# Kernel optimization log

Measured on AMD Instinct MI355X. Metric: run time of the kernel, lower is better.

## Reference

```python
import jax, jax.numpy as jnp
import numpy as np

B, S, D, H = 2, 2048, 2048, 16
DK = D // H  # 128


def _rope(x, cos, sin):
    # x: [B,S,H,DK]; pairs (x0,x1),(x2,x3),... rotated as complex numbers
    xr = x[..., 0::2]  # [B,S,H,DK/2]
    xi = x[..., 1::2]
    yr = xr * cos - xi * sin
    yi = xr * sin + xi * cos
    y = jnp.stack([yr, yi], axis=-1)  # [B,S,H,DK/2,2]
    return y.reshape(x.shape)


def setup_inputs() -> dict:
    key = jax.random.key(0)
    ks = jax.random.split(key, 12)
    sc = 1.0 / np.sqrt(D)
    q = jax.random.normal(ks[0], (B, S, D), jnp.float32)
    k = jax.random.normal(ks[1], (B, S, D), jnp.float32)
    v = jax.random.normal(ks[2], (B, S, D), jnp.float32)
    mask = jnp.tril(jnp.ones((S, S), jnp.int32))[None, None]  # causal [1,1,S,S]
    # standard RoPE angles: pos * theta^(-2i/dk)
    theta = 10000.0 ** (-jnp.arange(0, DK, 2, dtype=jnp.float32) / DK)  # [DK/2]
    freqs_angles = jnp.arange(S, dtype=jnp.float32)[:, None] * theta[None, :]  # [S,DK/2]
    wq = jax.random.normal(ks[3], (D, D), jnp.float32) * sc
    bq = jax.random.normal(ks[4], (D,), jnp.float32) * 0.01
    wk = jax.random.normal(ks[5], (D, D), jnp.float32) * sc
    bk = jax.random.normal(ks[6], (D,), jnp.float32) * 0.01
    wv = jax.random.normal(ks[7], (D, D), jnp.float32) * sc
    bv = jax.random.normal(ks[8], (D,), jnp.float32) * 0.01
    wo = jax.random.normal(ks[9], (D, D), jnp.float32) * sc
    bo = jax.random.normal(ks[10], (D,), jnp.float32) * 0.01
    return dict(q=q, k=k, v=v, mask=mask, freqs_angles=freqs_angles,
                wq=wq, bq=bq, wk=wk, bk=bk, wv=wv, bv=bv, wo=wo, bo=bo)


def reference(q, k, v, mask, freqs_angles, wq, bq, wk, bk, wv, bv, wo, bo):
    query = q @ wq.T + bq
    key_ = k @ wk.T + bk
    value = v @ wv.T + bv
    query = query.reshape(B, S, H, DK)
    key_ = key_.reshape(B, S, H, DK)
    value = value.reshape(B, S, H, DK).transpose(0, 2, 1, 3)  # [B,H,S,DK]
    cos = jnp.cos(freqs_angles)[None, :, None, :]  # [1,S,1,DK/2]
    sin = jnp.sin(freqs_angles)[None, :, None, :]
    query = _rope(query, cos, sin).transpose(0, 2, 1, 3)  # [B,H,S,DK]
    key_ = _rope(key_, cos, sin).transpose(0, 2, 1, 3)
    scores = jnp.einsum('bhqd,bhkd->bhqk', query, key_) / jnp.sqrt(jnp.float32(DK))
    scores = jnp.where(mask == 0, jnp.float32(-1e9), scores)
    attn = jax.nn.softmax(scores, axis=-1)  # dropout p=0.0 -> identity
    x = jnp.einsum('bhqk,bhkd->bhqd', attn, value)
    x = x.transpose(0, 2, 1, 3).reshape(B, S, D)
    return x @ wo.T + bo
```

## Files before the change

### kernel.cpp

```cpp
#include <hip/hip_runtime.h>
#include <hip/hip_bf16.h>

#define BB 2
#define SS 2048
#define DD 2048
#define HH 16
#define DKK 128
#define MM (BB*SS)

typedef unsigned short u16;
typedef short bf16x8 __attribute__((ext_vector_type(8)));
typedef unsigned short u16x8 __attribute__((ext_vector_type(8)));
typedef float f32x4 __attribute__((ext_vector_type(4)));

static __device__ __forceinline__ f32x4 mfma_bf16(bf16x8 a, bf16x8 b, f32x4 c) {
  return __builtin_amdgcn_mfma_f32_16x16x32_bf16(a, b, c, 0, 0, 0);
}

static __device__ __forceinline__ u16 f2b(float f) {
  unsigned int u = __float_as_uint(f);
  u = (u + 0x7FFFu + ((u >> 16) & 1u)) >> 16;
  return (u16)u;
}

static __device__ __forceinline__ u16 f2bq(float f) {
  unsigned int r;
  asm("v_cvt_pk_bf16_f32 %0, %1, %2" : "=v"(r) : "v"(f), "v"(f));
  return (u16)r;
}

static __device__ __forceinline__ void gl16(const u16* g, u16* l) {
  __builtin_amdgcn_global_load_lds(
      (const __attribute__((address_space(1))) unsigned int*)(const void*)g,
      (__attribute__((address_space(3))) unsigned int*)(void*)l, 16, 0, 0);
}

struct F2BArgs { const float* src[7]; u16* dst[7]; const float* fa; float* cs; };
__global__ __launch_bounds__(256) void k_f2bf_all(F2BArgs a) {
  int bid = blockIdx.x;
  if (bid >= 20480) {
    const int t0 = ((bid - 20480) * 256 + threadIdx.x) * 8;
    float4 a0 = *reinterpret_cast<const float4*>(a.fa + t0);
    float4 a1 = *reinterpret_cast<const float4*>(a.fa + t0 + 4);
    float4 o0, o1, o2, o3;
    o0.x = cosf(a0.x); o0.y = sinf(a0.x); o0.z = cosf(a0.y); o0.w = sinf(a0.y);
    o1.x = cosf(a0.z); o1.y = sinf(a0.z); o1.z = cosf(a0.w); o1.w = sinf(a0.w);
    o2.x = cosf(a1.x); o2.y = sinf(a1.x); o2.z = cosf(a1.y); o2.w = sinf(a1.y);
    o3.x = cosf(a1.z); o3.y = sinf(a1.z); o3.z = cosf(a1.w); o3.w = sinf(a1.w);
    float* out = a.cs + 2 * t0;
    *reinterpret_cast<float4*>(out)      = o0;
    *reinterpret_cast<float4*>(out + 4)  = o1;
    *reinterpret_cast<float4*>(out + 8)  = o2;
    *reinterpret_cast<float4*>(out + 12) = o3;
    return;
  }
  int buf, local;
  if (bid < 12288) { buf = bid >> 12; local = bid & 4095; }
  else { int t = bid - 12288; buf = 3 + (t >> 11); local = t & 2047; }
  const int i = (local * 256 + threadIdx.x) * 8;
  const float* in = a.src[buf];
  float4 v0 = *reinterpret_cast<const float4*>(in + i);
  float4 v1 = *reinterpret_cast<const float4*>(in + i + 4);
  u16x8 o;
  o[0]=f2b(v0.x); o[1]=f2b(v0.y); o[2]=f2b(v0.z); o[3]=f2b(v0.w);
  o[4]=f2b(v1.x); o[5]=f2b(v1.y); o[6]=f2b(v1.z); o[7]=f2b(v1.w);
  *reinterpret_cast<u16x8*>(a.dst[buf] + i) = o;
}

struct GemmJob { const u16* A; const u16* W; const float* bias; void* out; int mode; };
struct GemmArgs { GemmJob job[3]; };
__global__ __launch_bounds__(256, 2) void k_gemm(GemmArgs ga, const float* __restrict__ cs) {
  const GemmJob J = ga.job[blockIdx.z];
  const u16* __restrict__ A = J.A;
  const u16* __restrict__ W = J.W;
  const int mode = J.mode;
  const int K = DD, N = DD;

  __shared__ __align__(16) u16 sA[128 * 64];
  __shared__ __align__(16) u16 sB[256 * 64];
  const int tid = threadIdx.x;
  const int l  = tid & 63;
  const int w  = tid >> 6;
  const int wr = w >> 1;
  const int wc = w & 1;
  const int bm = blockIdx.x * 128, bn = blockIdx.y * 256;
  const int lr = l & 15;
  const int lg = l >> 4;

  f32x4 acc[4][8];
#pragma unroll
  for (int mi = 0; mi < 4; mi++)
#pragma unroll
    for (int ni = 0; ni < 8; ni++)
#pragma unroll
      for (int j = 0; j < 4; j++) acc[mi][ni][j] = 0.0f;

  const int srcx = ((l & 7) * 8) ^ ((l >> 3) * 8);
  const u16* gAl = A + (size_t)(bm + w*32 + (l >> 3)) * K + srcx;
  const u16* gBl = W + (size_t)(bn + w*64 + (l >> 3)) * K + srcx;

  const int rx = (lr & 7) * 8;

  for (int k0 = 0; k0 < K; k0 += 64) {
    __syncthreads();
#pragma unroll
    for (int i = 0; i < 4; i++) gl16(gAl + (size_t)i*8*K + k0, sA + (w*32 + i*8) * 64);
#pragma unroll
    for (int i = 0; i < 8; i++) gl16(gBl + (size_t)i*8*K + k0, sB + (w*64 + i*8) * 64);
    __syncthreads();

#pragma unroll
    for (int kk = 0; kk < 2; kk++) {
      bf16x8 af[4], bfv[8];
#pragma unroll
      for (int i = 0; i < 4; i++)
        af[i]  = *reinterpret_cast<const bf16x8*>(
            sA + (wr*64 + i*16 + lr) * 64 + ((kk*32 + lg*8) ^ rx));
#pragma unroll
      for (int i = 0; i < 8; i++)
        bfv[i] = *reinterpret_cast<const bf16x8*>(
            sB + (wc*128 + i*16 + lr) * 64 + ((kk*32 + lg*8) ^ rx));
#pragma unroll
      for (int mi = 0; mi < 4; mi++)
#pragma unroll
        for (int ni = 0; ni < 8; ni++)
          acc[mi][ni] = mfma_bf16(af[mi], bfv[ni], acc[mi][ni]);
    }
  }

#pragma unroll
  for (int mi = 0; mi < 4; mi++) {
#pragma unroll
    for (int ni = 0; ni < 8; ni++) {
      const int col = bn + wc*128 + ni*16 + lr;
      const float bv = J.bias[col];
#pragma unroll
      for (int r = 0; r < 4; r++) {
        const int row = bm + wr*64 + mi*16 + lg*4 + r;
        float v = acc[mi][ni][r] + bv;
        if (mode & 1) {
          const int s  = row & (SS - 1);
          const int dk = col & (DKK - 1);
          const int p  = dk >> 1;
          const float2 csv = *reinterpret_cast<const float2*>(cs + (size_t)(s*64 + p)*2);
          const float other = __shfl_xor(v, 1);
          const float sgn = (dk & 1) ? csv.y : -csv.y;
          v = v * csv.x + other * sgn;
          if (mode == 3) v *= 0.12751744f;
        }
        if (mode == 2) {
          reinterpret_cast<float*>(J.out)[(size_t)row * N + col] = v;
        } else {
          reinterpret_cast<u16*>(J.out)[(size_t)row * N + col] = f2b(v);
        }
      }
    }
  }
}

__global__ __launch_bounds__(256, 1) void k_attn(const u16* __restrict__ Qp,
                                                 const u16* __restrict__ Kp,
                                                 const u16* __restrict__ Vp,
                                                 u16* __restrict__ Op) {
  const int bid = blockIdx.x;
  const int qt = 15 - (bid >> 5);
  const int bh = bid & 31;
  const int h  = bh & 15;
  const int b  = bh >> 4;
  const int tid = threadIdx.x;
  const int l  = tid & 63, w = tid >> 6;
  const int lr = l & 15, lg = l >> 4;

  __shared__ __align__(16) u16 Klds[2 * 128 * 128];
  __shared__ __align__(16) u16 VT[128 * 128];
  __shared__ __align__(16) u16 PL[4][32][136];

  int koff[8];
#pragma unroll
  for (int i = 0; i < 8; i++) {
    const int row = w*32 + i*4 + (l >> 4);
    koff[i] = row * DD + (((l & 15) * 8) ^ ((row & 7) * 8));
  }
  const u16* kbase = Kp + (size_t)b * SS * DD + h * DKK;

  const int k0v = (tid >> 4) * 8;
  const int d0  = (tid & 15) * 8;
  const u16* vbase = Vp + (size_t)b * SS * DD + h * DKK + (size_t)k0v * DD + d0;

  uint4 vr[8];

  auto stageK = [&](int nk, int bufq) {
    const u16* kb = kbase + (size_t)nk * (128 * DD);
    u16* dst = Klds + bufq * 16384 + (w * 32) * 128;
#pragma unroll
    for (int i = 0; i < 8; i++) gl16(kb + koff[i], dst + i * 512);
  };
  auto prefV = [&](int nk) {
    const u16* vb = vbase + (size_t)nk * (128 * DD);
#pragma unroll
    for (int c = 0; c < 8; c++) vr[c] = *reinterpret_cast<const uint4*>(vb + c * DD);
  };

  int cur = 0;
  stageK(0, 0);
  prefV(0);

  bf16x8 qf[2][4];
#pragma unroll
  for (int mt = 0; mt < 2; mt++) {
    const size_t qrow = (size_t)(b*SS + qt*128 + w*32 + mt*16 + lr) * DD + h*DKK;
#pragma unroll
    for (int kk = 0; kk < 4; kk++)
      qf[mt][kk] = *reinterpret_cast<const bf16x8*>(Qp + qrow + kk*32 + lg*8);
  }

  float m[2][4], lsum[2][4];
  f32x4 oacc[2][8];
#pragma unroll
  for (int mt = 0; mt < 2; mt++)
#pragma unroll
    for (int r = 0; r < 4; r++) { m[mt][r] = -INFINITY; lsum[mt][r] = 0.0f; }
#pragma unroll
  for (int mt = 0; mt < 2; mt++)
#pragma unroll
    for (int dt = 0; dt < 8; dt++)
#pragma unroll
      for (int jj = 0; jj < 4; jj++) oacc[mt][dt][jj] = 0.0f;

#pragma unroll 1
  for (int kv = 0; kv <= qt; kv++) {
    __syncthreads();
#pragma unroll
    for (int dj = 0; dj < 8; dj++) {
      const int row = d0 + dj;
      const int col = k0v ^ (((row ^ (row >> 3)) & 15) * 8);
      u16x8 pk;
#pragma unroll
      for (int j = 0; j < 8; j++) pk[j] = reinterpret_cast<const u16*>(&vr[j])[dj];
      *reinterpret_cast<u16x8*>(VT + row * 128 + col) = pk;
    }
    __syncthreads();

    const bool hasnext = (kv < qt);
    if (hasnext) {
      prefV(kv + 1);
      stageK(kv + 1, cur ^ 1);
    }

    f32x4 sa[2][8];
#pragma unroll
    for (int mt = 0; mt < 2; mt++)
#pragma unroll
      for (int kt = 0; kt < 8; kt++)
#pragma unroll
        for (int jj = 0; jj < 4; jj++) sa[mt][kt][jj] = 0.0f;
    const u16* kl = Klds + cur * 16384;
    __builtin_amdgcn_s_setprio(1);
#pragma unroll
    for (int kk = 0; kk < 4; kk++) {
#pragma unroll
      for (int kt = 0; kt < 8; kt++) {
        const int row = kt*16 + lr;
        const bf16x8 kf = *reinterpret_cast<const bf16x8*>(
            kl + row * 128 + ((kk*32 + lg*8) ^ ((row & 7) * 8)));
#pragma unroll
        for (int mt = 0; mt < 2; mt++)
          sa[mt][kt] = mfma_bf16(qf[mt][kk], kf, sa[mt][kt]);
      }
    }
    __builtin_amdgcn_s_setprio(0);

    if (kv == qt) {
#pragma unroll
      for (int kt = 0; kt < 8; kt++) {
        const int key = kv*128 + kt*16 + lr;
#pragma unroll
        for (int mt = 0; mt < 2; mt++)
#pragma unroll
          for (int r = 0; r < 4; r++) {
            const int qv = qt*128 + w*32 + mt*16 + lg*4 + r;
            if (key > qv) sa[mt][kt][r] = -1e9f;
          }
      }
    }

    float pm[2][4];
#pragma unroll
    for (int mt = 0; mt < 2; mt++)
#pragma unroll
      for (int r = 0; r < 4; r++) {
        float t0 = fmaxf(fmaxf(sa[mt][0][r], sa[mt][1][r]), fmaxf(sa[mt][2][r], sa[mt][3][r]));
        float t1 = fmaxf(fmaxf(sa[mt][4][r], sa[mt][5][r]), fmaxf(sa[mt][6][r], sa[mt][7][r]));
        pm[mt][r] = fmaxf(t0, t1);
      }
    bool ok = true;
#pragma unroll
    for (int mt = 0; mt < 2; mt++)
#pragma unroll
      for (int r = 0; r < 4; r++) ok = ok && (pm[mt][r] <= m[mt][r] + 8.0f);
    if (!__all(ok)) {
#pragma unroll
      for (int mt = 0; mt < 2; mt++)
#pragma unroll
        for (int r = 0; r < 4; r++) {
          float t = pm[mt][r];
#pragma unroll
          for (int d = 1; d < 16; d <<= 1) t = fmaxf(t, __shfl_xor(t, d));
          const float mnew = fmaxf(m[mt][r], t);
          const float corr = exp2f(m[mt][r] - mnew);
          lsum[mt][r] *= corr;
#pragma unroll
          for (int dt = 0; dt < 8; dt++) oacc[mt][dt][r] *= corr;
          m[mt][r] = mnew;
        }
    }

#pragma unroll
    for (int mt = 0; mt < 2; mt++)
#pragma unroll
      for (int r = 0; r < 4; r++) {
        float rs = 0.0f;
#pragma unroll
        for (int kt = 0; kt < 8; kt++) {
          const float e = exp2f(sa[mt][kt][r] - m[mt][r]);
          rs += e;
          PL[w][mt*16 + lg*4 + r][kt*16 + lr] = f2bq(e);
        }
        lsum[mt][r] += rs;
      }

    __builtin_amdgcn_s_setprio(1);
#pragma unroll
    for (int kk2 = 0; kk2 < 4; kk2++) {
      bf16x8 pa[2];
#pragma unroll
      for (int mt = 0; mt < 2; mt++)
        pa[mt] = *reinterpret_cast<const bf16x8*>(&PL[w][mt*16 + lr][kk2*32 + lg*8]);
#pragma unroll
      for (int dt = 0; dt < 8; dt++) {
        const int row = dt*16 + lr;
        const bf16x8 vb = *reinterpret_cast<const bf16x8*>(
            VT + row * 128 + ((kk2*32 + lg*8) ^ (((row ^ (row >> 3)) & 15) * 8)));
#pragma unroll
        for (int mt = 0; mt < 2; mt++)
          oacc[mt][dt] = mfma_bf16(pa[mt], vb, oacc[mt][dt]);
      }
    }
    __builtin_amdgcn_s_setprio(0);

    if (hasnext) cur ^= 1;
  }

  float inv[2][4];
#pragma unroll
  for (int mt = 0; mt < 2; mt++)
#pragma unroll
    for (int r = 0; r < 4; r++) {
      float t = lsum[mt][r];
#pragma unroll
      for (int d = 1; d < 16; d <<= 1) t += __shfl_xor(t, d);
      inv[mt][r] = 1.0f / t;
    }
#pragma unroll
  for (int mt = 0; mt < 2; mt++)
#pragma unroll
    for (int dt = 0; dt < 8; dt++)
#pragma unroll
      for (int r = 0; r < 4; r++) {
        const size_t row = (size_t)(b*SS + qt*128 + w*32 + mt*16 + lg*4 + r);
        Op[row * DD + h*DKK + dt*16 + lr] = f2bq(oacc[mt][dt][r] * inv[mt][r]);
      }
}

extern "C" void kernel_launch(void* const* d_in, const int* in_sizes, int n_in,
                              void* d_out, int out_size, void* d_ws, size_t ws_size,
                              hipStream_t stream) {
  const float* q  = (const float*)d_in[0];
  const float* k  = (const float*)d_in[1];
  const float* v  = (const float*)d_in[2];
  const float* fa = (const float*)d_in[4];
  const float* wq = (const float*)d_in[5];
  const float* bq = (const float*)d_in[6];
  const float* wk = (const float*)d_in[7];
  const float* bk = (const float*)d_in[8];
  const float* wv = (const float*)d_in[9];
  const float* bv = (const float*)d_in[10];
  const float* wo = (const float*)d_in[11];
  const float* bo = (const float*)d_in[12];

  float* cs = (float*)d_ws;
  u16* bf = (u16*)((char*)d_ws + (size_t)262144 * sizeof(float));
  const size_t NX = (size_t)MM * DD;
  const size_t NW = (size_t)DD * DD;
  u16* q_bf  = bf;
  u16* k_bf  = q_bf + NX;
  u16* v_bf  = k_bf + NX;
  u16* wq_bf = v_bf + NX;
  u16* wk_bf = wq_bf + NW;
  u16* wv_bf = wk_bf + NW;
  u16* wo_bf = wv_bf + NW;
  u16* Qp    = wo_bf + NW;
  u16* Kp    = Qp + NX;
  u16* Vp    = Kp + NX;
  u16* Ao    = Vp + NX;

  F2BArgs fa7;
  fa7.src[0] = q;  fa7.dst[0] = q_bf;
  fa7.src[1] = k;  fa7.dst[1] = k_bf;
  fa7.src[2] = v;  fa7.dst[2] = v_bf;
  fa7.src[3] = wq; fa7.dst[3] = wq_bf;
  fa7.src[4] = wk; fa7.dst[4] = wk_bf;
  fa7.src[5] = wv; fa7.dst[5] = wv_bf;
  fa7.src[6] = wo; fa7.dst[6] = wo_bf;
  fa7.fa = fa;     fa7.cs = cs;
  k_f2bf_all<<<dim3(20544), 256, 0, stream>>>(fa7);

  GemmArgs gq;
  gq.job[0] = GemmJob{ q_bf, wq_bf, bq, (void*)Qp, 3 };
  gq.job[1] = GemmJob{ k_bf, wk_bf, bk, (void*)Kp, 1 };
  gq.job[2] = GemmJob{ v_bf, wv_bf, bv, (void*)Vp, 0 };
  k_gemm<<<dim3(MM/128, DD/256, 3), 256, 0, stream>>>(gq, cs);

  k_attn<<<dim3(512), 256, 0, stream>>>(Qp, Kp, Vp, Ao);

  GemmArgs go;
  go.job[0] = GemmJob{ Ao, wo_bf, bo, d_out, 2 };
  go.job[1] = go.job[0];
  go.job[2] = go.job[0];
  k_gemm<<<dim3(MM/128, DD/256, 1), 256, 0, stream>>>(go, cs);
}
```

Measured before the change: 344.8 us.

## Halve attention KV tile, raise occupancy, reorder blocks, add 128x128 output GEMM

The attention kernel now processes 64-key tiles instead of 128, cutting LDS and register use so two blocks can share a CU (launch bounds 2). Blocks are split into heavy-first and light-first halves to balance the causal workload. The output projection switches to a new 128x128-tile GEMM, which launches twice as many blocks for better CU fill. The trade-off is more loop iterations and barriers per attention block, and less data reuse per tile in the output GEMM.

```diff
diff --git a/kernel.cpp b/kernel.cpp
--- a/kernel.cpp
+++ b/kernel.cpp
@@ -69,6 +69,7 @@
 
 struct GemmJob { const u16* A; const u16* W; const float* bias; void* out; int mode; };
 struct GemmArgs { GemmJob job[3]; };
+
 __global__ __launch_bounds__(256, 2) void k_gemm(GemmArgs ga, const float* __restrict__ cs) {
   const GemmJob J = ga.job[blockIdx.z];
   const u16* __restrict__ A = J.A;
@@ -158,47 +159,136 @@
   }
 }
 
-__global__ __launch_bounds__(256, 1) void k_attn(const u16* __restrict__ Qp,
+__global__ __launch_bounds__(256) void k_gemm3(GemmArgs ga, const float* __restrict__ cs) {
+  const GemmJob J = ga.job[blockIdx.z];
+  const u16* __restrict__ A = J.A;
+  const u16* __restrict__ W = J.W;
+  const int mode = J.mode;
+  const int K = DD, N = DD;
+
+  __shared__ __align__(16) u16 sA[128 * 64];
+  __shared__ __align__(16) u16 sB[128 * 64];
+  const int tid = threadIdx.x;
+  const int l  = tid & 63;
+  const int w  = tid >> 6;
+  const int wr = w >> 1, wc = w & 1;
+  const int bm = blockIdx.x * 128, bn = blockIdx.y * 128;
+  const int lr = l & 15;
+  const int lg = l >> 4;
+
+  f32x4 acc[4][4];
+#pragma unroll
+  for (int mi = 0; mi < 4; mi++)
+#pragma unroll
+    for (int ni = 0; ni < 4; ni++)
+#pragma unroll
+      for (int j = 0; j < 4; j++) acc[mi][ni][j] = 0.0f;
+
+  const int srcx = ((l & 7) * 8) ^ ((l >> 3) * 8);
+  const u16* gAl = A + (size_t)(bm + w*32 + (l >> 3)) * K + srcx;
+  const u16* gBl = W + (size_t)(bn + w*32 + (l >> 3)) * K + srcx;
+
+  const int rx = (lr & 7) * 8;
+
+  for (int k0 = 0; k0 < K; k0 += 64) {
+    __syncthreads();
+#pragma unroll
+    for (int i = 0; i < 4; i++) gl16(gAl + (size_t)i*8*K + k0, sA + (w*32 + i*8) * 64);
+#pragma unroll
+    for (int i = 0; i < 4; i++) gl16(gBl + (size_t)i*8*K + k0, sB + (w*32 + i*8) * 64);
+    __syncthreads();
+
+#pragma unroll
+    for (int kk = 0; kk < 2; kk++) {
+      bf16x8 af[4], bfv[4];
+#pragma unroll
+      for (int i = 0; i < 4; i++)
+        af[i]  = *reinterpret_cast<const bf16x8*>(
+            sA + (wr*64 + i*16 + lr) * 64 + ((kk*32 + lg*8) ^ rx));
+#pragma unroll
+      for (int i = 0; i < 4; i++)
+        bfv[i] = *reinterpret_cast<const bf16x8*>(
+            sB + (wc*64 + i*16 + lr) * 64 + ((kk*32 + lg*8) ^ rx));
+#pragma unroll
+      for (int mi = 0; mi < 4; mi++)
+#pragma unroll
+        for (int ni = 0; ni < 4; ni++)
+          acc[mi][ni] = mfma_bf16(af[mi], bfv[ni], acc[mi][ni]);
+    }
+  }
+
+#pragma unroll
+  for (int mi = 0; mi < 4; mi++) {
+#pragma unroll
+    for (int ni = 0; ni < 4; ni++) {
+      const int col = bn + wc*64 + ni*16 + lr;
+      const float bv = J.bias[col];
+#pragma unroll
+      for (int r = 0; r < 4; r++) {
+        const int row = bm + wr*64 + mi*16 + lg*4 + r;
+        float v = acc[mi][ni][r] + bv;
+        if (mode & 1) {
+          const int s  = row & (SS - 1);
+          const int dk = col & (DKK - 1);
+          const int p  = dk >> 1;
+          const float2 csv = *reinterpret_cast<const float2*>(cs + (size_t)(s*64 + p)*2);
+          const float other = __shfl_xor(v, 1);
+          const float sgn = (dk & 1) ? csv.y : -csv.y;
+          v = v * csv.x + other * sgn;
+          if (mode == 3) v *= 0.12751744f;
+        }
+        if (mode == 2) {
+          reinterpret_cast<float*>(J.out)[(size_t)row * N + col] = v;
+        } else {
+          reinterpret_cast<u16*>(J.out)[(size_t)row * N + col] = f2b(v);
+        }
+      }
+    }
+  }
+}
+
+__global__ __launch_bounds__(256, 2) void k_attn(const u16* __restrict__ Qp,
                                                  const u16* __restrict__ Kp,
                                                  const u16* __restrict__ Vp,
                                                  u16* __restrict__ Op) {
   const int bid = blockIdx.x;
-  const int qt = 15 - (bid >> 5);
-  const int bh = bid & 31;
+  int bh, qt;
+  if (bid < 256) { bh = bid & 31; qt = 15 - (bid >> 5); }
+  else { int b2 = bid - 256; bh = b2 & 31; qt = b2 >> 5; }
   const int h  = bh & 15;
   const int b  = bh >> 4;
   const int tid = threadIdx.x;
   const int l  = tid & 63, w = tid >> 6;
   const int lr = l & 15, lg = l >> 4;
 
-  __shared__ __align__(16) u16 Klds[2 * 128 * 128];
-  __shared__ __align__(16) u16 VT[128 * 128];
-  __shared__ __align__(16) u16 PL[4][32][136];
-
-  int koff[8];
-#pragma unroll
-  for (int i = 0; i < 8; i++) {
-    const int row = w*32 + i*4 + (l >> 4);
+  __shared__ __align__(16) u16 Klds[2 * 64 * 128];
+  __shared__ __align__(16) u16 VT[128 * 64];
+  __shared__ __align__(16) u16 PL[4][32][72];
+
+  int koff[4];
+#pragma unroll
+  for (int i = 0; i < 4; i++) {
+    const int row = w*16 + i*4 + (l >> 4);
     koff[i] = row * DD + (((l & 15) * 8) ^ ((row & 7) * 8));
   }
   const u16* kbase = Kp + (size_t)b * SS * DD + h * DKK;
 
-  const int k0v = (tid >> 4) * 8;
-  const int d0  = (tid & 15) * 8;
+  const int k0v = (tid >> 5) * 8;
+  const int d0  = (tid & 31) * 4;
   const u16* vbase = Vp + (size_t)b * SS * DD + h * DKK + (size_t)k0v * DD + d0;
 
-  uint4 vr[8];
+  uint2 vr[8];
 
   auto stageK = [&](int nk, int bufq) {
-    const u16* kb = kbase + (size_t)nk * (128 * DD);
-    u16* dst = Klds + bufq * 16384 + (w * 32) * 128;
-#pragma unroll
-    for (int i = 0; i < 8; i++) gl16(kb + koff[i], dst + i * 512);
+    const u16* kb = kbase + (size_t)nk * (64 * DD);
+    u16* dst = Klds + bufq * 8192 + (w * 16) * 128;
+#pragma unroll
+    for (int i = 0; i < 4; i++) gl16(kb + koff[i], dst + i * 512);
   };
   auto prefV = [&](int nk) {
-    const u16* vb = vbase + (size_t)nk * (128 * DD);
-#pragma unroll
-    for (int c = 0; c < 8; c++) vr[c] = *reinterpret_cast<const uint4*>(vb + c * DD);
+    const u16* vb = vbase + (size_t)nk * (64 * DD);
+#pragma unroll
+    for (int c = 0; c < 8; c++) vr[c] = *reinterpret_cast<const uint2*>(vb + c * DD);
   };
 
   int cur = 0;
@@ -227,39 +317,40 @@
 #pragma unroll
       for (int jj = 0; jj < 4; jj++) oacc[mt][dt][jj] = 0.0f;
 
+  const int kvmax = 2 * qt + 1;
 #pragma unroll 1
-  for (int kv = 0; kv <= qt; kv++) {
+  for (int kv = 0; kv <= kvmax; kv++) {
     __syncthreads();
 #pragma unroll
-    for (int dj = 0; dj < 8; dj++) {
+    for (int dj = 0; dj < 4; dj++) {
       const int row = d0 + dj;
-      const int col = k0v ^ (((row ^ (row >> 3)) & 15) * 8);
+      const int col = k0v ^ (((row ^ (row >> 3)) & 7) * 8);
       u16x8 pk;
 #pragma unroll
       for (int j = 0; j < 8; j++) pk[j] = reinterpret_cast<const u16*>(&vr[j])[dj];
-      *reinterpret_cast<u16x8*>(VT + row * 128 + col) = pk;
+      *reinterpret_cast<u16x8*>(VT + row * 64 + col) = pk;
     }
     __syncthreads();
 
-    const bool hasnext = (kv < qt);
+    const bool hasnext = (kv < kvmax);
     if (hasnext) {
       prefV(kv + 1);
       stageK(kv + 1, cur ^ 1);
     }
 
-    f32x4 sa[2][8];
+    f32x4 sa[2][4];
 #pragma unroll
     for (int mt = 0; mt < 2; mt++)
 #pragma unroll
-      for (int kt = 0; kt < 8; kt++)
+      for (int kt = 0; kt < 4; kt++)
 #pragma unroll
         for (int jj = 0; jj < 4; jj++) sa[mt][kt][jj] = 0.0f;
-    const u16* kl = Klds + cur * 16384;
+    const u16* kl = Klds + cur * 8192;
     __builtin_amdgcn_s_setprio(1);
 #pragma unroll
     for (int kk = 0; kk < 4; kk++) {
 #pragma unroll
-      for (int kt = 0; kt < 8; kt++) {
+      for (int kt = 0; kt < 4; kt++) {
         const int row = kt*16 + lr;
         const bf16x8 kf = *reinterpret_cast<const bf16x8*>(
             kl + row * 128 + ((kk*32 + lg*8) ^ ((row & 7) * 8)));
@@ -270,10 +361,10 @@
     }
     __builtin_amdgcn_s_setprio(0);
 
-    if (kv == qt) {
-#pragma unroll
-      for (int kt = 0; kt < 8; kt++) {
-        const int key = kv*128 + kt*16 + lr;
+    if (kv >= 2 * qt) {
+#pragma unroll
+      for (int kt = 0; kt < 4; kt++) {
+        const int key = kv*64 + kt*16 + lr;
 #pragma unroll
         for (int mt = 0; mt < 2; mt++)
 #pragma unroll
@@ -288,11 +379,9 @@
 #pragma unroll
     for (int mt = 0; mt < 2; mt++)
 #pragma unroll
-      for (int r = 0; r < 4; r++) {
-        float t0 = fmaxf(fmaxf(sa[mt][0][r], sa[mt][1][r]), fmaxf(sa[mt][2][r], sa[mt][3][r]));
-        float t1 = fmaxf(fmaxf(sa[mt][4][r], sa[mt][5][r]), fmaxf(sa[mt][6][r], sa[mt][7][r]));
-        pm[mt][r] = fmaxf(t0, t1);
-      }
+      for (int r = 0; r < 4; r++)
+        pm[mt][r] = fmaxf(fmaxf(sa[mt][0][r], sa[mt][1][r]),
+                          fmaxf(sa[mt][2][r], sa[mt][3][r]));
     bool ok = true;
 #pragma unroll
     for (int mt = 0; mt < 2; mt++)
@@ -321,7 +410,7 @@
       for (int r = 0; r < 4; r++) {
         float rs = 0.0f;
 #pragma unroll
-        for (int kt = 0; kt < 8; kt++) {
+        for (int kt = 0; kt < 4; kt++) {
           const float e = exp2f(sa[mt][kt][r] - m[mt][r]);
           rs += e;
           PL[w][mt*16 + lg*4 + r][kt*16 + lr] = f2bq(e);
@@ -331,7 +420,7 @@
 
     __builtin_amdgcn_s_setprio(1);
 #pragma unroll
-    for (int kk2 = 0; kk2 < 4; kk2++) {
+    for (int kk2 = 0; kk2 < 2; kk2++) {
       bf16x8 pa[2];
 #pragma unroll
       for (int mt = 0; mt < 2; mt++)
@@ -340,7 +429,7 @@
       for (int dt = 0; dt < 8; dt++) {
         const int row = dt*16 + lr;
         const bf16x8 vb = *reinterpret_cast<const bf16x8*>(
-            VT + row * 128 + ((kk2*32 + lg*8) ^ (((row ^ (row >> 3)) & 15) * 8)));
+            VT + row * 64 + ((kk2*32 + lg*8) ^ (((row ^ (row >> 3)) & 7) * 8)));
 #pragma unroll
         for (int mt = 0; mt < 2; mt++)
           oacc[mt][dt] = mfma_bf16(pa[mt], vb, oacc[mt][dt]);
@@ -427,5 +516,5 @@
   go.job[0] = GemmJob{ Ao, wo_bf, bo, d_out, 2 };
   go.job[1] = go.job[0];
   go.job[2] = go.job[0];
-  k_gemm<<<dim3(MM/128, DD/256, 1), 256, 0, stream>>>(go, cs);
-}
+  k_gemm3<<<dim3(MM/128, DD/128, 1), 256, 0, stream>>>(go, cs);
+}
```

New measurement: 316.6 us. 8.2% less time.
